# Performance work log

Hardware: AMD Instinct MI355X
Metric: run time of the kernel (lower is better)

## Reference

```python
import jax, jax.numpy as jnp
import numpy as np

B, T, D = 32, 1024, 192
HIDDEN = 4
CH = D * HIDDEN          # conv hidden channels = in_channel * hidden_size
K1, K2 = 5, 3
PAD = 3                  # (K1 - 1) // 2 + 1 for odd kernel_size=5 (ReplicationPad1d)
NUM_LEVELS = 3
N_NODES = 2 ** NUM_LEVELS - 1  # 7 Interaction blocks in the SCINet tree
OUT_LEN = 512


def setup_inputs() -> dict:
    key = jax.random.key(0)
    ks = jax.random.split(key, 6)
    s1 = 1.0 / np.sqrt(D * K1)   # torch Conv1d default init bound (fan_in = Cin*k)
    s2 = 1.0 / np.sqrt(CH * K2)
    sp = 1.0 / np.sqrt(T)
    x = jax.random.normal(ks[0], (B, T, D), dtype=jnp.float32)
    # Stacked params for all 7 tree nodes x 4 branches (phi, psi, eta, rho)
    W1 = jax.random.uniform(ks[1], (N_NODES, 4, CH, D, K1), jnp.float32, -s1, s1)
    b1 = jax.random.uniform(ks[2], (N_NODES, 4, CH), jnp.float32, -s1, s1)
    W2 = jax.random.uniform(ks[3], (N_NODES, 4, D, CH, K2), jnp.float32, -s2, s2)
    b2 = jax.random.uniform(ks[4], (N_NODES, 4, D), jnp.float32, -s2, s2)
    # projection1 = Conv1d(input_len, output_len, k=1, bias=False) over time-as-channels
    Wproj = jax.random.uniform(ks[5], (OUT_LEN, T), jnp.float32, -sp, sp)
    return {"x": x, "W1": W1, "b1": b1, "W2": W2, "b2": b2, "Wproj": Wproj}


def _conv1d(x, w, b):
    # x: (B, Cin, L), w: (Cout, Cin, K)
    y = jax.lax.conv_general_dilated(x, w, (1,), 'VALID',
                                     dimension_numbers=('NCH', 'OIH', 'NCH'))
    return y + b[None, :, None]


def _branch(x, w1, b1, w2, b2):
    # ReplicationPad1d(3,3) -> Conv(k=5) -> LeakyReLU -> (Dropout p=0) -> Conv(k=3) -> Tanh
    xp = jnp.pad(x, ((0, 0), (0, 0), (PAD, PAD)), mode='edge')
    h = jax.nn.leaky_relu(_conv1d(xp, w1, b1), 0.01)
    return jnp.tanh(_conv1d(h, w2, b2))  # length back to L


def _interact(x, w1, b1, w2, b2):
    # x: (B, T, D) -> even/odd (B, D, T/2)
    xe = jnp.transpose(x[:, ::2, :], (0, 2, 1))
    xo = jnp.transpose(x[:, 1::2, :], (0, 2, 1))
    d = xo * jnp.exp(_branch(xe, w1[0], b1[0], w2[0], b2[0]))  # phi
    c = xe * jnp.exp(_branch(xo, w1[1], b1[1], w2[1], b2[1]))  # psi
    even_up = c + _branch(d, w1[2], b1[2], w2[2], b2[2])        # eta
    odd_up = d - _branch(c, w1[3], b1[3], w2[3], b2[3])         # rho
    return jnp.transpose(even_up, (0, 2, 1)), jnp.transpose(odd_up, (0, 2, 1))


def _zip_up(even, odd):
    # interleave even/odd along time (equal lengths since T % 2**levels == 0)
    b, t, c = even.shape
    return jnp.stack([even, odd], axis=2).reshape(b, 2 * t, c)


def _tree(x, level, idx, W1, b1, W2, b2):
    i = idx[0]
    idx[0] += 1
    e, o = _interact(x, W1[i], b1[i], W2[i], b2[i])
    if level == 0:
        return _zip_up(e, o)
    return _zip_up(_tree(e, level - 1, idx, W1, b1, W2, b2),
                   _tree(o, level - 1, idx, W1, b1, W2, b2))


def reference(x, W1, b1, W2, b2, Wproj):
    out = _tree(x, NUM_LEVELS - 1, [0], W1, b1, W2, b2) + x  # residual
    # projection1: Conv1d over time-as-channels, kernel 1, no bias
    return jnp.einsum('btd,ot->bod', out, Wproj)
```

## Files before the change

kernel.cpp:

```cpp
#include <hip/hip_runtime.h>
#include <hip/hip_bf16.h>

typedef unsigned short u16;
typedef unsigned int u32;
typedef __bf16 bf16x8 __attribute__((ext_vector_type(8)));
typedef float f32x4 __attribute__((ext_vector_type(4)));

#define NB 32
#define NT 1024
#define ND 192
#define NCH 768
#define NOUT 512

__device__ __forceinline__ float bf2f(u16 x) { return __uint_as_float(((u32)x) << 16); }
__device__ __forceinline__ u16 f2bf(float f) {
    u32 u = __float_as_uint(f);
    return (u16)((u + 0x7fffu + ((u >> 16) & 1u)) >> 16);
}
__device__ __forceinline__ float tanh_fast(float x) {
    float e = __expf(2.f * x);
    return 1.f - 2.f / (e + 1.f);
}
__device__ __forceinline__ int xcd_swz(int bx, int nwg) {
    int q = nwg >> 3, r = nwg & 7;
    int xcd = bx & 7, idx = bx >> 3;
    return (xcd < r ? xcd * (q + 1) : r * (q + 1) + (xcd - r) * q) + idx;
}

__constant__ int NODE_IDX[3][4] = {{0, 0, 0, 0}, {1, 4, 0, 0}, {2, 5, 3, 6}};

__global__ void cvt8(const float* __restrict__ in, u16* __restrict__ out, int n8) {
    int i = blockIdx.x * 256 + threadIdx.x;
    if (i >= n8) return;
    const float4* p = (const float4*)in + 2 * (size_t)i;
    float4 a = p[0], c = p[1];
    uint4 o;
    o.x = f2bf(a.x) | ((u32)f2bf(a.y) << 16);
    o.y = f2bf(a.z) | ((u32)f2bf(a.w) << 16);
    o.z = f2bf(c.x) | ((u32)f2bf(c.y) << 16);
    o.w = f2bf(c.z) | ((u32)f2bf(c.w) << 16);
    ((uint4*)out)[i] = o;
}

__global__ __launch_bounds__(256) void w1fk(const float* __restrict__ W1, u16* __restrict__ W1f) {
    __shared__ u16 ls[32][968];
    const int nb = blockIdx.x / 24;
    const int cot = blockIdx.x % 24;
    const float* src = W1 + ((size_t)nb * NCH + cot * 32) * (ND * 5);
    for (int idx = threadIdx.x; idx < 7680; idx += 256) {
        int e4 = idx * 4;
        int rowc = e4 / 960, col = e4 % 960;
        float4 v = *(const float4*)(src + (size_t)rowc * 960 + col);
        ls[rowc][col + 0] = f2bf(v.x);
        ls[rowc][col + 1] = f2bf(v.y);
        ls[rowc][col + 2] = f2bf(v.z);
        ls[rowc][col + 3] = f2bf(v.w);
    }
    __syncthreads();
    const int lane = threadIdx.x & 63, sub = threadIdx.x >> 6;
    const int g = lane >> 4, r = lane & 15;
    for (int it = 0; it < 15; ++it) {
        int fid = it * 4 + sub;
        int kkb = fid >> 1, cobl = fid & 1;
        u16 tmp[8];
#pragma unroll
        for (int e = 0; e < 8; ++e) {
            int kk = kkb * 32 + 8 * g + e;
            int ci = kk % 192, k = kk / 192;
            tmp[e] = ls[cobl * 16 + r][ci * 5 + k];
        }
        uint4 o;
        o.x = tmp[0] | ((u32)tmp[1] << 16);
        o.y = tmp[2] | ((u32)tmp[3] << 16);
        o.z = tmp[4] | ((u32)tmp[5] << 16);
        o.w = tmp[6] | ((u32)tmp[7] << 16);
        size_t off = (((size_t)nb * 30 + kkb) * 48 + cot * 2 + cobl) * 512 + lane * 8;
        *(uint4*)(W1f + off) = o;
    }
}

__global__ __launch_bounds__(256) void w2fk(const float* __restrict__ W2, u16* __restrict__ W2f) {
    __shared__ u16 ls[16][1160];
    const int ch = blockIdx.x & 1;
    const int t = blockIdx.x >> 1;
    const int nb = t / 12, cot = t % 12;
    const float* src = W2 + ((size_t)nb * ND + cot * 16) * (NCH * 3) + ch * 1152;
    for (int idx = threadIdx.x; idx < 4608; idx += 256) {
        int e4 = idx * 4;
        int rowc = e4 / 1152, col = e4 % 1152;
        float4 v = *(const float4*)(src + (size_t)rowc * (NCH * 3) + col);
        ls[rowc][col + 0] = f2bf(v.x);
        ls[rowc][col + 1] = f2bf(v.y);
        ls[rowc][col + 2] = f2bf(v.z);
        ls[rowc][col + 3] = f2bf(v.w);
    }
    __syncthreads();
    const int lane = threadIdx.x & 63, sub = threadIdx.x >> 6;
    const int g = lane >> 4, r = lane & 15;
    for (int it = 0; it < 9; ++it) {
        int fid = it * 4 + sub;
        int k = fid / 12, cib = fid % 12;
        int kkb = k * 24 + ch * 12 + cib;
        u16 tmp[8];
#pragma unroll
        for (int e = 0; e < 8; ++e) {
            int cl = cib * 32 + 8 * g + e;
            tmp[e] = ls[r][cl * 3 + k];
        }
        uint4 o;
        o.x = tmp[0] | ((u32)tmp[1] << 16);
        o.y = tmp[2] | ((u32)tmp[3] << 16);
        o.z = tmp[4] | ((u32)tmp[5] << 16);
        o.w = tmp[6] | ((u32)tmp[7] << 16);
        size_t off = (((size_t)nb * 72 + kkb) * 12 + cot) * 512 + lane * 8;
        *(uint4*)(W2f + off) = o;
    }
}

__global__ __launch_bounds__(256) void conv1m(
    const u16* __restrict__ bufb, const u16* __restrict__ dbufb, const u16* __restrict__ cbufb,
    const u16* __restrict__ W1f, const float* __restrict__ b1,
    u16* __restrict__ h, int lvl, int stage) {
    const int L = 512 >> lvl, nodes = 1 << lvl, Lout = L + 2;
    const int tid = threadIdx.x;
    const int mT1 = (NB * Lout + 63) / 64;
    const int wg = xcd_swz(blockIdx.x, gridDim.x);
    const int z = wg / (6 * mT1);
    const int rem = wg - z * 6 * mT1;
    const int mt = rem / 6;
    const int cot = rem % 6;
    const int g_node = z & (nodes - 1);
    const int br = z >> lvl;
    const int nb4 = NODE_IDX[lvl][g_node] * 4 + (stage ? 2 + br : br);

    const int r0 = mt * 64;
    const int b0 = r0 / Lout;
    const int t00 = r0 - b0 * Lout;
    const int s = Lout - t00;
    const int rowsValid0 = NB * Lout - r0;
    const int rowsValid = rowsValid0 < 64 ? rowsValid0 : 64;

    __shared__ u16 xs[72 * 192];

    const u16* dcb = br ? cbufb : dbufb;
    const int slot = g_node + (br << lvl);
    for (int ch = tid; ch < 72 * 24; ch += 256) {
        int j = ch / 24, c8 = ch % 24;
        int bb, u;
        if (j <= s + 3) { bb = b0; u = t00 - 3 + j; }
        else            { bb = b0 + 1; u = j - s - 7; }
        u = u < 0 ? 0 : (u > L - 1 ? L - 1 : u);
        if (bb > NB - 1) bb = NB - 1;
        const u16* p;
        if (stage == 0)
            p = bufb + ((size_t)bb * NT + slot + (size_t)u * (2 * nodes)) * ND + c8 * 8;
        else
            p = dcb + (((size_t)g_node * NB + bb) * L + u) * (size_t)ND + c8 * 8;
        *(uint4*)(xs + j * 192 + ((c8 * 8) ^ ((j & 7) << 3))) = *(const uint4*)p;
    }
    __syncthreads();

    const int lane = tid & 63, w = tid >> 6;
    const int lr = lane & 15, lg = lane >> 4;

    int rowb[4];
#pragma unroll
    for (int m = 0; m < 4; ++m) {
        int i = m * 16 + lr;
        rowb[m] = i + (i >= s ? 4 : 0);
    }
    const u16* wf = W1f + (size_t)nb4 * 30 * 48 * 512 + (size_t)(cot * 8 + w * 2) * 512 + lane * 8;

    f32x4 acc[4][2];
    f32x4 zz = {0.f, 0.f, 0.f, 0.f};
#pragma unroll
    for (int m = 0; m < 4; ++m)
#pragma unroll
        for (int n = 0; n < 2; ++n) acc[m][n] = zz;

    auto loadA = [&](bf16x8(&dst)[4], int step) {
        const int k = step / 6, cib = step % 6;
#pragma unroll
        for (int m = 0; m < 4; ++m) {
            int row = rowb[m] + k;
            int idx = row * 192 + ((cib * 32 + lg * 8) ^ ((row & 7) << 3));
            dst[m] = *(const bf16x8*)(xs + idx);
        }
    };
    auto loadB = [&](bf16x8(&dst)[2], int step) {
#pragma unroll
        for (int n = 0; n < 2; ++n)
            dst[n] = *(const bf16x8*)(wf + ((size_t)step * 48 + n) * 512);
    };
    auto domfma = [&](bf16x8(&A)[4], bf16x8(&B)[2]) {
#pragma unroll
        for (int m = 0; m < 4; ++m)
#pragma unroll
            for (int n = 0; n < 2; ++n)
                acc[m][n] = __builtin_amdgcn_mfma_f32_16x16x32_bf16(A[m], B[n], acc[m][n], 0, 0, 0);
    };

    bf16x8 Ab[2][4], Bb[3][2];
    loadA(Ab[0], 0);
    loadB(Bb[0], 0);
    loadB(Bb[1], 1);
#pragma unroll
    for (int sp = 0; sp < 30; ++sp) {
        if (sp + 2 < 30) loadB(Bb[(sp + 2) % 3], sp + 2);
        if (sp + 1 < 30) loadA(Ab[(sp + 1) & 1], sp + 1);
        domfma(Ab[sp & 1], Bb[sp % 3]);
    }

    float bias[2];
    const float* bb1 = b1 + (size_t)nb4 * NCH + cot * 128 + w * 32 + lr;
#pragma unroll
    for (int n = 0; n < 2; ++n) bias[n] = bb1[n * 16];
    u16* hz = h + (size_t)z * NB * Lout * NCH;
#pragma unroll
    for (int m = 0; m < 4; ++m) {
#pragma unroll
        for (int rr = 0; rr < 4; ++rr) {
            int i = m * 16 + lg * 4 + rr;
            if (i < rowsValid) {
                int cross = (i >= s) ? 1 : 0;
                int bb = b0 + cross;
                int tt = cross ? i - s : t00 + i;
                u16* dst = hz + ((size_t)bb * Lout + tt) * NCH + cot * 128 + w * 32 + lr;
#pragma unroll
                for (int n = 0; n < 2; ++n) {
                    float v = acc[m][n][rr] + bias[n];
                    v = v > 0.f ? v : 0.01f * v;
                    dst[n * 16] = f2bf(v);
                }
            }
        }
    }
}

__global__ __launch_bounds__(256) void conv2m(
    u16* __restrict__ bufb, u16* __restrict__ dbufb, u16* __restrict__ cbufb,
    const u16* __restrict__ W2f, const float* __restrict__ b2,
    const u16* __restrict__ h, int lvl, int stage) {
    const int L = 512 >> lvl, nodes = 1 << lvl, Lout = L + 2;
    const int tid = threadIdx.x;
    const int nM = (NB * L) >> 6;
    const int wg = xcd_swz(blockIdx.x, gridDim.x);
    const int z = wg / (nM * 2);
    const int rem = wg - z * nM * 2;
    const int mt = rem >> 1;
    const int nh = rem & 1;
    const int g_node = z & (nodes - 1);
    const int br = z >> lvl;
    const int nb4 = NODE_IDX[lvl][g_node] * 4 + (stage ? 2 + br : br);
    const int r0 = mt * 64;
    const int b = r0 >> (9 - lvl);
    const int t0 = r0 & (L - 1);

    __shared__ u16 xs[66 * 192];
    const u16* hz = h + ((size_t)z * NB + b) * Lout * NCH;

    const int lane = tid & 63, w = tid >> 6;
    const int wrow = w >> 1, wcol = w & 1;
    const int lr = lane & 15, lg = lane >> 4;
    int rowb[2];
#pragma unroll
    for (int m = 0; m < 2; ++m) rowb[m] = wrow * 32 + m * 16 + lr;
    const u16* wf = W2f + (size_t)nb4 * 72 * 12 * 512 + (size_t)(nh * 6 + wcol * 3) * 512 + lane * 8;

    f32x4 acc[2][3];
    f32x4 zz = {0.f, 0.f, 0.f, 0.f};
#pragma unroll
    for (int m = 0; m < 2; ++m)
#pragma unroll
        for (int n = 0; n < 3; ++n) acc[m][n] = zz;

    for (int cc = 0; cc < 4; ++cc) {
        __syncthreads();
        for (int ch = tid; ch < 66 * 24; ch += 256) {
            int j = ch / 24, c8 = ch % 24;
            *(uint4*)(xs + j * 192 + ((c8 * 8) ^ ((j & 7) << 3))) =
                *(const uint4*)(hz + (size_t)(t0 + j) * NCH + cc * 192 + c8 * 8);
        }
        __syncthreads();

        auto loadA = [&](bf16x8(&dst)[2], int step) {
            const int k = step / 6, cib = step % 6;
#pragma unroll
            for (int m = 0; m < 2; ++m) {
                int row = rowb[m] + k;
                int idx = row * 192 + ((cib * 32 + lg * 8) ^ ((row & 7) << 3));
                dst[m] = *(const bf16x8*)(xs + idx);
            }
        };
        auto loadB = [&](bf16x8(&dst)[3], int step) {
            const int k = step / 6, cib = step % 6;
            const size_t kb = (size_t)(cc * 6 + k * 24 + cib) * 12 * 512;
#pragma unroll
            for (int n = 0; n < 3; ++n)
                dst[n] = *(const bf16x8*)(wf + kb + (size_t)n * 512);
        };
        auto domfma = [&](bf16x8(&A)[2], bf16x8(&B)[3]) {
#pragma unroll
            for (int m = 0; m < 2; ++m)
#pragma unroll
                for (int n = 0; n < 3; ++n)
                    acc[m][n] = __builtin_amdgcn_mfma_f32_16x16x32_bf16(A[m], B[n], acc[m][n], 0, 0, 0);
        };

        bf16x8 Ab[2][2], Bb[3][3];
        loadA(Ab[0], 0);
        loadB(Bb[0], 0);
        loadB(Bb[1], 1);
#pragma unroll
        for (int sp = 0; sp < 18; ++sp) {
            if (sp + 2 < 18) loadB(Bb[(sp + 2) % 3], sp + 2);
            if (sp + 1 < 18) loadA(Ab[(sp + 1) & 1], sp + 1);
            domfma(Ab[sp & 1], Bb[sp % 3]);
        }
    }

    float bias[3];
    const float* bb2 = b2 + (size_t)nb4 * ND + nh * 96 + wcol * 48 + lr;
#pragma unroll
    for (int n = 0; n < 3; ++n) bias[n] = bb2[n * 16];

    const int tstr = 2 * nodes;
    if (stage == 0) {
        const int mo = g_node + (br == 0 ? nodes : 0);
        const u16* mult = bufb + ((size_t)b * NT + mo) * ND;
        u16* dst = (br == 0 ? dbufb : cbufb) + ((size_t)g_node * NB + b) * (size_t)L * ND;
#pragma unroll
        for (int m = 0; m < 2; ++m) {
#pragma unroll
            for (int rr = 0; rr < 4; ++rr) {
                int i = wrow * 32 + m * 16 + lg * 4 + rr;
                int t = t0 + i;
#pragma unroll
                for (int n = 0; n < 3; ++n) {
                    int co = nh * 96 + wcol * 48 + n * 16 + lr;
                    float v = tanh_fast(acc[m][n][rr] + bias[n]);
                    float mlt = bf2f(mult[(size_t)t * tstr * ND + co]);
                    dst[(size_t)t * ND + co] = f2bf(mlt * __expf(v));
                }
            }
        }
    } else {
        const u16* other = (br == 0 ? cbufb : dbufb) + ((size_t)g_node * NB + b) * (size_t)L * ND;
        const int to = g_node + (br ? nodes : 0);
        u16* dst = bufb + ((size_t)b * NT + to) * ND;
#pragma unroll
        for (int m = 0; m < 2; ++m) {
#pragma unroll
            for (int rr = 0; rr < 4; ++rr) {
                int i = wrow * 32 + m * 16 + lg * 4 + rr;
                int t = t0 + i;
#pragma unroll
                for (int n = 0; n < 3; ++n) {
                    int co = nh * 96 + wcol * 48 + n * 16 + lr;
                    float v = tanh_fast(acc[m][n][rr] + bias[n]);
                    float o = bf2f(other[(size_t)t * ND + co]);
                    dst[(size_t)t * tstr * ND + co] = f2bf(br == 0 ? o + v : o - v);
                }
            }
        }
    }
}

__global__ __launch_bounds__(256) void mkin2T(const u16* __restrict__ bufb,
                                              const float* __restrict__ x,
                                              u16* __restrict__ in2T) {
    __shared__ u16 ls[64][72];
    const int b = blockIdx.z, t0 = blockIdx.y * 64, d0 = blockIdx.x * 64;
    const int tid = threadIdx.x;
#pragma unroll
    for (int it = 0; it < 2; ++it) {
        int idx = tid + it * 256;
        int c8 = idx >> 6, row = idx & 63;
        size_t base = ((size_t)b * NT + t0 + row) * ND + d0 + c8 * 8;
        uint4 vb = *(const uint4*)(bufb + base);
        float4 x1 = *(const float4*)(x + base);
        float4 x2 = *(const float4*)(x + base + 4);
        const u16* vs = (const u16*)&vb;
        ls[c8 * 8 + 0][row] = f2bf(bf2f(vs[0]) + x1.x);
        ls[c8 * 8 + 1][row] = f2bf(bf2f(vs[1]) + x1.y);
        ls[c8 * 8 + 2][row] = f2bf(bf2f(vs[2]) + x1.z);
        ls[c8 * 8 + 3][row] = f2bf(bf2f(vs[3]) + x1.w);
        ls[c8 * 8 + 4][row] = f2bf(bf2f(vs[4]) + x2.x);
        ls[c8 * 8 + 5][row] = f2bf(bf2f(vs[5]) + x2.y);
        ls[c8 * 8 + 6][row] = f2bf(bf2f(vs[6]) + x2.z);
        ls[c8 * 8 + 7][row] = f2bf(bf2f(vs[7]) + x2.w);
    }
    __syncthreads();
#pragma unroll
    for (int it = 0; it < 2; ++it) {
        int idx = tid + it * 256;
        int dl = idx >> 3, t8 = idx & 7;
        uint4 v = *(uint4*)&ls[dl][t8 * 8];
        *(uint4*)(in2T + ((size_t)b * ND + d0 + dl) * NT + t0 + t8 * 8) = v;
    }
}

__global__ __launch_bounds__(256) void projm(const u16* __restrict__ in2T,
                                             const u16* __restrict__ Wpb,
                                             float* __restrict__ out) {
    const int b = blockIdx.y, ot = blockIdx.x;
    const int tid = threadIdx.x, lane = tid & 63, w = tid >> 6;
    const int lr = lane & 15, lg = lane >> 4;
    const u16* ap = Wpb + ((size_t)(ot * 32 + lr)) * NT + lg * 8;
    const u16* bp = in2T + ((size_t)b * ND + w * 48 + lr) * NT + lg * 8;

    f32x4 acc[2][3];
    f32x4 zz = {0.f, 0.f, 0.f, 0.f};
#pragma unroll
    for (int m = 0; m < 2; ++m)
#pragma unroll
        for (int n = 0; n < 3; ++n) acc[m][n] = zz;

    auto loadA = [&](bf16x8(&dst)[2], int kkb) {
#pragma unroll
        for (int m = 0; m < 2; ++m)
            dst[m] = *(const bf16x8*)(ap + (size_t)m * 16 * NT + kkb * 32);
    };
    auto loadB = [&](bf16x8(&dst)[3], int kkb) {
#pragma unroll
        for (int n = 0; n < 3; ++n)
            dst[n] = *(const bf16x8*)(bp + (size_t)n * 16 * NT + kkb * 32);
    };
    auto domfma = [&](bf16x8(&A)[2], bf16x8(&B)[3]) {
#pragma unroll
        for (int m = 0; m < 2; ++m)
#pragma unroll
            for (int n = 0; n < 3; ++n)
                acc[m][n] = __builtin_amdgcn_mfma_f32_16x16x32_bf16(A[m], B[n], acc[m][n], 0, 0, 0);
    };

    bf16x8 Ab[2][2], Bb[3][3];
    loadA(Ab[0], 0);
    loadB(Bb[0], 0);
    loadB(Bb[1], 1);
#pragma unroll
    for (int sp = 0; sp < 32; ++sp) {
        if (sp + 2 < 32) loadB(Bb[(sp + 2) % 3], sp + 2);
        if (sp + 1 < 32) loadA(Ab[(sp + 1) & 1], sp + 1);
        domfma(Ab[sp & 1], Bb[sp % 3]);
    }

#pragma unroll
    for (int m = 0; m < 2; ++m)
#pragma unroll
        for (int rr = 0; rr < 4; ++rr) {
            int o = ot * 32 + m * 16 + lg * 4 + rr;
#pragma unroll
            for (int n = 0; n < 3; ++n) {
                int d = w * 48 + n * 16 + lr;
                out[((size_t)b * NOUT + o) * ND + d] = acc[m][n][rr];
            }
        }
}

extern "C" void kernel_launch(void* const* d_in, const int* in_sizes, int n_in,
                              void* d_out, int out_size, void* d_ws, size_t ws_size,
                              hipStream_t stream) {
    const float* x = (const float*)d_in[0];
    const float* W1 = (const float*)d_in[1];
    const float* b1 = (const float*)d_in[2];
    const float* W2 = (const float*)d_in[3];
    const float* b2 = (const float*)d_in[4];
    const float* Wp = (const float*)d_in[5];
    float* out = (float*)d_out;

    char* wsb = (char*)d_ws;
    size_t off = 0;
    auto carve = [&](size_t bytes) {
        void* p = wsb + off;
        off += (bytes + 255) & ~(size_t)255;
        return p;
    };
    const size_t w1f_e = (size_t)28 * 30 * 48 * 512;
    const size_t w2f_e = (size_t)28 * 72 * 12 * 512;
    const size_t wpb_e = (size_t)NOUT * NT;
    const size_t buf_e = (size_t)NB * NT * ND;
    const size_t dc_e = (size_t)NB * 512 * ND;
    const size_t h_e = (size_t)1040 * NB * NCH;
    const size_t i2_e = (size_t)NB * ND * NT;

    u16* W1f = (u16*)carve(sizeof(u16) * w1f_e);
    u16* W2f = (u16*)carve(sizeof(u16) * w2f_e);
    u16* Wpb = (u16*)carve(sizeof(u16) * wpb_e);
    u16* bufb = (u16*)carve(sizeof(u16) * buf_e);
    u16* dbufb = (u16*)carve(sizeof(u16) * dc_e);
    u16* cbufb = (u16*)carve(sizeof(u16) * dc_e);
    u16* h = (u16*)carve(sizeof(u16) * h_e);
    u16* in2T = (u16*)carve(sizeof(u16) * i2_e);
    if (off > ws_size) return;

    cvt8<<<(int)(buf_e / 8 / 256), 256, 0, stream>>>(x, bufb, (int)(buf_e / 8));
    cvt8<<<(int)(wpb_e / 8 / 256), 256, 0, stream>>>(Wp, Wpb, (int)(wpb_e / 8));
    w1fk<<<28 * 24, 256, 0, stream>>>(W1, W1f);
    w2fk<<<28 * 12 * 2, 256, 0, stream>>>(W2, W2f);

    for (int lvl = 0; lvl < 3; ++lvl) {
        int L = 512 >> lvl, nodes = 1 << lvl, Lout = L + 2;
        int mT1 = (NB * Lout + 63) / 64;
        int nM = NB * L / 64;
        dim3 g1(6 * mT1 * 2 * nodes);
        dim3 g2(nM * 2 * 2 * nodes);
        conv1m<<<g1, 256, 0, stream>>>(bufb, dbufb, cbufb, W1f, b1, h, lvl, 0);
        conv2m<<<g2, 256, 0, stream>>>(bufb, dbufb, cbufb, W2f, b2, h, lvl, 0);
        conv1m<<<g1, 256, 0, stream>>>(bufb, dbufb, cbufb, W1f, b1, h, lvl, 1);
        conv2m<<<g2, 256, 0, stream>>>(bufb, dbufb, cbufb, W2f, b2, h, lvl, 1);
    }
    mkin2T<<<dim3(3, 16, NB), 256, 0, stream>>>(bufb, x, in2T);
    projm<<<dim3(16, NB), 256, 0, stream>>>(in2T, Wpb, out);
}
```

Measured before the change: 778.4 us.

## Enlarge conv tiles to 128 rows with 512-thread blocks

Both conv kernels move to 512-thread workgroups with 128-row M tiles. In conv1 each weight fragment is now shared across two warp rows, and conv2 drops its N-half split so one block covers all 192 output channels, with a deeper 4-stage weight prefetch that runs across the channel chunks. This cuts redundant global weight and activation loads per output, at the cost of more shared memory, more registers per thread and fewer workgroups, which may hurt occupancy and load balance at the deeper tree levels.

```diff
diff --git a/kernel.cpp b/kernel.cpp
--- a/kernel.cpp
+++ b/kernel.cpp
@@ -117,13 +117,13 @@
     }
 }
 
-__global__ __launch_bounds__(256) void conv1m(
+__global__ __launch_bounds__(512) void conv1m(
     const u16* __restrict__ bufb, const u16* __restrict__ dbufb, const u16* __restrict__ cbufb,
     const u16* __restrict__ W1f, const float* __restrict__ b1,
     u16* __restrict__ h, int lvl, int stage) {
     const int L = 512 >> lvl, nodes = 1 << lvl, Lout = L + 2;
     const int tid = threadIdx.x;
-    const int mT1 = (NB * Lout + 63) / 64;
+    const int mT1 = (NB * Lout + 127) / 128;
     const int wg = xcd_swz(blockIdx.x, gridDim.x);
     const int z = wg / (6 * mT1);
     const int rem = wg - z * 6 * mT1;
@@ -133,18 +133,33 @@
     const int br = z >> lvl;
     const int nb4 = NODE_IDX[lvl][g_node] * 4 + (stage ? 2 + br : br);
 
-    const int r0 = mt * 64;
+    const int r0 = mt * 128;
     const int b0 = r0 / Lout;
     const int t00 = r0 - b0 * Lout;
     const int s = Lout - t00;
     const int rowsValid0 = NB * Lout - r0;
-    const int rowsValid = rowsValid0 < 64 ? rowsValid0 : 64;
-
-    __shared__ u16 xs[72 * 192];
+    const int rowsValid = rowsValid0 < 128 ? rowsValid0 : 128;
+
+    __shared__ u16 xs[136 * 192];
+
+    const int lane = tid & 63, w = tid >> 6;
+    const int wrow = w >> 2, wcol = w & 3;
+    const int lr = lane & 15, lg = lane >> 4;
+    const u16* wf = W1f + ((size_t)nb4 * 30 * 48 + cot * 8 + wcol * 2) * 512 + lane * 8;
+
+    bf16x8 Bb[4][2], Ab[2][4];
+    auto loadB = [&](bf16x8(&dst)[2], int step) {
+#pragma unroll
+        for (int n = 0; n < 2; ++n)
+            dst[n] = *(const bf16x8*)(wf + ((size_t)step * 48 + n) * 512);
+    };
+    loadB(Bb[0], 0);
+    loadB(Bb[1], 1);
+    loadB(Bb[2], 2);
 
     const u16* dcb = br ? cbufb : dbufb;
     const int slot = g_node + (br << lvl);
-    for (int ch = tid; ch < 72 * 24; ch += 256) {
+    for (int ch = tid; ch < 136 * 24; ch += 512) {
         int j = ch / 24, c8 = ch % 24;
         int bb, u;
         if (j <= s + 3) { bb = b0; u = t00 - 3 + j; }
@@ -160,16 +175,12 @@
     }
     __syncthreads();
 
-    const int lane = tid & 63, w = tid >> 6;
-    const int lr = lane & 15, lg = lane >> 4;
-
     int rowb[4];
 #pragma unroll
     for (int m = 0; m < 4; ++m) {
-        int i = m * 16 + lr;
+        int i = wrow * 64 + m * 16 + lr;
         rowb[m] = i + (i >= s ? 4 : 0);
     }
-    const u16* wf = W1f + (size_t)nb4 * 30 * 48 * 512 + (size_t)(cot * 8 + w * 2) * 512 + lane * 8;
 
     f32x4 acc[4][2];
     f32x4 zz = {0.f, 0.f, 0.f, 0.f};
@@ -183,36 +194,24 @@
 #pragma unroll
         for (int m = 0; m < 4; ++m) {
             int row = rowb[m] + k;
-            int idx = row * 192 + ((cib * 32 + lg * 8) ^ ((row & 7) << 3));
-            dst[m] = *(const bf16x8*)(xs + idx);
-        }
-    };
-    auto loadB = [&](bf16x8(&dst)[2], int step) {
-#pragma unroll
-        for (int n = 0; n < 2; ++n)
-            dst[n] = *(const bf16x8*)(wf + ((size_t)step * 48 + n) * 512);
-    };
-    auto domfma = [&](bf16x8(&A)[4], bf16x8(&B)[2]) {
+            dst[m] = *(const bf16x8*)(xs + row * 192 + ((cib * 32 + lg * 8) ^ ((row & 7) << 3)));
+        }
+    };
+    loadA(Ab[0], 0);
+#pragma unroll
+    for (int st = 0; st < 30; ++st) {
+        if (st + 3 < 30) loadB(Bb[(st + 3) & 3], st + 3);
+        if (st + 1 < 30) loadA(Ab[(st + 1) & 1], st + 1);
 #pragma unroll
         for (int m = 0; m < 4; ++m)
 #pragma unroll
             for (int n = 0; n < 2; ++n)
-                acc[m][n] = __builtin_amdgcn_mfma_f32_16x16x32_bf16(A[m], B[n], acc[m][n], 0, 0, 0);
-    };
-
-    bf16x8 Ab[2][4], Bb[3][2];
-    loadA(Ab[0], 0);
-    loadB(Bb[0], 0);
-    loadB(Bb[1], 1);
-#pragma unroll
-    for (int sp = 0; sp < 30; ++sp) {
-        if (sp + 2 < 30) loadB(Bb[(sp + 2) % 3], sp + 2);
-        if (sp + 1 < 30) loadA(Ab[(sp + 1) & 1], sp + 1);
-        domfma(Ab[sp & 1], Bb[sp % 3]);
+                acc[m][n] = __builtin_amdgcn_mfma_f32_16x16x32_bf16(
+                    Ab[st & 1][m], Bb[st & 3][n], acc[m][n], 0, 0, 0);
     }
 
     float bias[2];
-    const float* bb1 = b1 + (size_t)nb4 * NCH + cot * 128 + w * 32 + lr;
+    const float* bb1 = b1 + (size_t)nb4 * NCH + cot * 128 + wcol * 32 + lr;
 #pragma unroll
     for (int n = 0; n < 2; ++n) bias[n] = bb1[n * 16];
     u16* hz = h + (size_t)z * NB * Lout * NCH;
@@ -220,12 +219,12 @@
     for (int m = 0; m < 4; ++m) {
 #pragma unroll
         for (int rr = 0; rr < 4; ++rr) {
-            int i = m * 16 + lg * 4 + rr;
+            int i = wrow * 64 + m * 16 + lg * 4 + rr;
             if (i < rowsValid) {
                 int cross = (i >= s) ? 1 : 0;
                 int bb = b0 + cross;
                 int tt = cross ? i - s : t00 + i;
-                u16* dst = hz + ((size_t)bb * Lout + tt) * NCH + cot * 128 + w * 32 + lr;
+                u16* dst = hz + ((size_t)bb * Lout + tt) * NCH + cot * 128 + wcol * 32 + lr;
 #pragma unroll
                 for (int n = 0; n < 2; ++n) {
                     float v = acc[m][n][rr] + bias[n];
@@ -237,90 +236,86 @@
     }
 }
 
-__global__ __launch_bounds__(256) void conv2m(
+__global__ __launch_bounds__(512) void conv2m(
     u16* __restrict__ bufb, u16* __restrict__ dbufb, u16* __restrict__ cbufb,
     const u16* __restrict__ W2f, const float* __restrict__ b2,
     const u16* __restrict__ h, int lvl, int stage) {
     const int L = 512 >> lvl, nodes = 1 << lvl, Lout = L + 2;
     const int tid = threadIdx.x;
-    const int nM = (NB * L) >> 6;
+    const int nM = (NB * L) >> 7;
     const int wg = xcd_swz(blockIdx.x, gridDim.x);
-    const int z = wg / (nM * 2);
-    const int rem = wg - z * nM * 2;
-    const int mt = rem >> 1;
-    const int nh = rem & 1;
+    const int z = wg / nM;
+    const int mt = wg - z * nM;
     const int g_node = z & (nodes - 1);
     const int br = z >> lvl;
     const int nb4 = NODE_IDX[lvl][g_node] * 4 + (stage ? 2 + br : br);
-    const int r0 = mt * 64;
+    const int r0 = mt * 128;
     const int b = r0 >> (9 - lvl);
     const int t0 = r0 & (L - 1);
 
-    __shared__ u16 xs[66 * 192];
+    __shared__ u16 xs[130 * 192];
     const u16* hz = h + ((size_t)z * NB + b) * Lout * NCH;
 
     const int lane = tid & 63, w = tid >> 6;
-    const int wrow = w >> 1, wcol = w & 1;
+    const int wrow = w >> 2, wcol = w & 3;
     const int lr = lane & 15, lg = lane >> 4;
-    int rowb[2];
-#pragma unroll
-    for (int m = 0; m < 2; ++m) rowb[m] = wrow * 32 + m * 16 + lr;
-    const u16* wf = W2f + (size_t)nb4 * 72 * 12 * 512 + (size_t)(nh * 6 + wcol * 3) * 512 + lane * 8;
-
-    f32x4 acc[2][3];
+    const u16* wf = W2f + ((size_t)nb4 * 72 * 12 + wcol * 3) * 512 + lane * 8;
+
+    auto kkb_of = [](int st) {
+        int cc = st / 18, sp = st % 18;
+        return (sp / 6) * 24 + cc * 6 + (sp % 6);
+    };
+    bf16x8 Bb[4][3], Ab[2][4];
+    auto loadB = [&](bf16x8(&dst)[3], int st) {
+        const size_t kb = (size_t)kkb_of(st) * 12 * 512;
+#pragma unroll
+        for (int n = 0; n < 3; ++n)
+            dst[n] = *(const bf16x8*)(wf + kb + (size_t)n * 512);
+    };
+    auto loadA = [&](bf16x8(&dst)[4], int sp) {
+        const int k = sp / 6, cj = sp % 6;
+#pragma unroll
+        for (int m = 0; m < 4; ++m) {
+            int row = wrow * 64 + m * 16 + lr + k;
+            dst[m] = *(const bf16x8*)(xs + row * 192 + ((cj * 32 + lg * 8) ^ ((row & 7) << 3)));
+        }
+    };
+    loadB(Bb[0], 0);
+    loadB(Bb[1], 1);
+    loadB(Bb[2], 2);
+
+    f32x4 acc[4][3];
     f32x4 zz = {0.f, 0.f, 0.f, 0.f};
 #pragma unroll
-    for (int m = 0; m < 2; ++m)
+    for (int m = 0; m < 4; ++m)
 #pragma unroll
         for (int n = 0; n < 3; ++n) acc[m][n] = zz;
 
     for (int cc = 0; cc < 4; ++cc) {
         __syncthreads();
-        for (int ch = tid; ch < 66 * 24; ch += 256) {
+        for (int ch = tid; ch < 130 * 24; ch += 512) {
             int j = ch / 24, c8 = ch % 24;
             *(uint4*)(xs + j * 192 + ((c8 * 8) ^ ((j & 7) << 3))) =
                 *(const uint4*)(hz + (size_t)(t0 + j) * NCH + cc * 192 + c8 * 8);
         }
         __syncthreads();
-
-        auto loadA = [&](bf16x8(&dst)[2], int step) {
-            const int k = step / 6, cib = step % 6;
-#pragma unroll
-            for (int m = 0; m < 2; ++m) {
-                int row = rowb[m] + k;
-                int idx = row * 192 + ((cib * 32 + lg * 8) ^ ((row & 7) << 3));
-                dst[m] = *(const bf16x8*)(xs + idx);
-            }
-        };
-        auto loadB = [&](bf16x8(&dst)[3], int step) {
-            const int k = step / 6, cib = step % 6;
-            const size_t kb = (size_t)(cc * 6 + k * 24 + cib) * 12 * 512;
-#pragma unroll
-            for (int n = 0; n < 3; ++n)
-                dst[n] = *(const bf16x8*)(wf + kb + (size_t)n * 512);
-        };
-        auto domfma = [&](bf16x8(&A)[2], bf16x8(&B)[3]) {
-#pragma unroll
-            for (int m = 0; m < 2; ++m)
+        loadA(Ab[0], 0);
+#pragma unroll
+        for (int sp = 0; sp < 18; ++sp) {
+            int st = cc * 18 + sp;
+            if (st + 3 < 72) loadB(Bb[(st + 3) & 3], st + 3);
+            if (sp + 1 < 18) loadA(Ab[(sp + 1) & 1], sp + 1);
+#pragma unroll
+            for (int m = 0; m < 4; ++m)
 #pragma unroll
                 for (int n = 0; n < 3; ++n)
-                    acc[m][n] = __builtin_amdgcn_mfma_f32_16x16x32_bf16(A[m], B[n], acc[m][n], 0, 0, 0);
-        };
-
-        bf16x8 Ab[2][2], Bb[3][3];
-        loadA(Ab[0], 0);
-        loadB(Bb[0], 0);
-        loadB(Bb[1], 1);
-#pragma unroll
-        for (int sp = 0; sp < 18; ++sp) {
-            if (sp + 2 < 18) loadB(Bb[(sp + 2) % 3], sp + 2);
-            if (sp + 1 < 18) loadA(Ab[(sp + 1) & 1], sp + 1);
-            domfma(Ab[sp & 1], Bb[sp % 3]);
+                    acc[m][n] = __builtin_amdgcn_mfma_f32_16x16x32_bf16(
+                        Ab[sp & 1][m], Bb[st & 3][n], acc[m][n], 0, 0, 0);
         }
     }
 
     float bias[3];
-    const float* bb2 = b2 + (size_t)nb4 * ND + nh * 96 + wcol * 48 + lr;
+    const float* bb2 = b2 + (size_t)nb4 * ND + wcol * 48 + lr;
 #pragma unroll
     for (int n = 0; n < 3; ++n) bias[n] = bb2[n * 16];
 
@@ -330,14 +325,14 @@
         const u16* mult = bufb + ((size_t)b * NT + mo) * ND;
         u16* dst = (br == 0 ? dbufb : cbufb) + ((size_t)g_node * NB + b) * (size_t)L * ND;
 #pragma unroll
-        for (int m = 0; m < 2; ++m) {
+        for (int m = 0; m < 4; ++m) {
 #pragma unroll
             for (int rr = 0; rr < 4; ++rr) {
-                int i = wrow * 32 + m * 16 + lg * 4 + rr;
+                int i = wrow * 64 + m * 16 + lg * 4 + rr;
                 int t = t0 + i;
 #pragma unroll
                 for (int n = 0; n < 3; ++n) {
-                    int co = nh * 96 + wcol * 48 + n * 16 + lr;
+                    int co = wcol * 48 + n * 16 + lr;
                     float v = tanh_fast(acc[m][n][rr] + bias[n]);
                     float mlt = bf2f(mult[(size_t)t * tstr * ND + co]);
                     dst[(size_t)t * ND + co] = f2bf(mlt * __expf(v));
@@ -349,14 +344,14 @@
         const int to = g_node + (br ? nodes : 0);
         u16* dst = bufb + ((size_t)b * NT + to) * ND;
 #pragma unroll
-        for (int m = 0; m < 2; ++m) {
+        for (int m = 0; m < 4; ++m) {
 #pragma unroll
             for (int rr = 0; rr < 4; ++rr) {
-                int i = wrow * 32 + m * 16 + lg * 4 + rr;
+                int i = wrow * 64 + m * 16 + lg * 4 + rr;
                 int t = t0 + i;
 #pragma unroll
                 for (int n = 0; n < 3; ++n) {
-                    int co = nh * 96 + wcol * 48 + n * 16 + lr;
+                    int co = wcol * 48 + n * 16 + lr;
                     float v = tanh_fast(acc[m][n][rr] + bias[n]);
                     float o = bf2f(other[(size_t)t * ND + co]);
                     dst[(size_t)t * tstr * ND + co] = f2bf(br == 0 ? o + v : o - v);
@@ -501,14 +496,14 @@
 
     for (int lvl = 0; lvl < 3; ++lvl) {
         int L = 512 >> lvl, nodes = 1 << lvl, Lout = L + 2;
-        int mT1 = (NB * Lout + 63) / 64;
-        int nM = NB * L / 64;
+        int mT1 = (NB * Lout + 127) / 128;
+        int nM = NB * L / 128;
         dim3 g1(6 * mT1 * 2 * nodes);
-        dim3 g2(nM * 2 * 2 * nodes);
-        conv1m<<<g1, 256, 0, stream>>>(bufb, dbufb, cbufb, W1f, b1, h, lvl, 0);
-        conv2m<<<g2, 256, 0, stream>>>(bufb, dbufb, cbufb, W2f, b2, h, lvl, 0);
-        conv1m<<<g1, 256, 0, stream>>>(bufb, dbufb, cbufb, W1f, b1, h, lvl, 1);
-        conv2m<<<g2, 256, 0, stream>>>(bufb, dbufb, cbufb, W2f, b2, h, lvl, 1);
+        dim3 g2(nM * 2 * nodes);
+        conv1m<<<g1, 512, 0, stream>>>(bufb, dbufb, cbufb, W1f, b1, h, lvl, 0);
+        conv2m<<<g2, 512, 0, stream>>>(bufb, dbufb, cbufb, W2f, b2, h, lvl, 0);
+        conv1m<<<g1, 512, 0, stream>>>(bufb, dbufb, cbufb, W1f, b1, h, lvl, 1);
+        conv2m<<<g2, 512, 0, stream>>>(bufb, dbufb, cbufb, W2f, b2, h, lvl, 1);
     }
     mkin2T<<<dim3(3, 16, NB), 256, 0, stream>>>(bufb, x, in2T);
     projm<<<dim3(16, NB), 256, 0, stream>>>(in2T, Wpb, out);
```

Result: slower. 1.320 ms (+69.6%).
